# Kernel optimization log

Measured on AMD Instinct MI355X. Metric: run time of the kernel, lower is better.

The kernel has to match this reference:

```python
import jax, jax.numpy as jnp
import numpy as np

B, H, W, P = 32, 512, 512, 8192
EPS = 1e-5


def setup_inputs() -> dict:
    key = jax.random.key(0)
    k1, k2, k3, k4, k5 = jax.random.split(key, 5)
    return {
        "depth_3dmm": jax.random.normal(k1, (B, 1, H, W), jnp.float32),
        "depth_pigan": jax.random.normal(k2, (B, 1, H, W), jnp.float32),
        "mask": jax.random.randint(k3, (B, 1, H, W), 0, 2, jnp.int32),
        "sample1_raw": jax.random.randint(k4, (B, P), 0, H * W, jnp.int32),
        "sample2_raw": jax.random.randint(k5, (B, P), 0, H * W, jnp.int32),
    }


def reference(depth_3dmm, depth_pigan, mask, sample1_raw, sample2_raw):
    d3 = depth_3dmm.squeeze(axis=1)   # [B,H,W]
    dp = depth_pigan.squeeze(axis=1)  # [B,H,W]
    m = mask[:, 0].astype(bool)       # [B,H,W]
    Bv = m.shape[0]

    # Emulate torch.masked_select compaction with a fixed-shape stable argsort:
    # valid elements come first, in flat row-major order (same as masked_select).
    mflat = m.reshape(-1)
    order = jnp.argsort(jnp.logical_not(mflat))  # stable by default
    d3c = d3.reshape(-1)[order]  # compacted depth_3dmm (padding at tail)
    dpc = dp.reshape(-1)[order]  # compacted depth_pigan

    valid_num = m.reshape(Bv, -1).sum(axis=1)          # [B]
    batch_base = jnp.cumsum(valid_num) - valid_num     # [B]

    s1 = (sample1_raw % valid_num[:, None] + batch_base[:, None]).reshape(-1)
    s2 = (sample2_raw % valid_num[:, None] + batch_base[:, None]).reshape(-1)

    diff = dpc[s1] - dpc[s2]
    a, b = d3c[s1], d3c[s2]
    gt = a > b + EPS
    lt = a < b - EPS

    # mean(relu(-diff)[gt]) and mean(relu(diff)[lt]) without dynamic shapes
    loss1 = jnp.where(gt, jax.nn.relu(-diff), 0.0).sum() / gt.sum()
    loss2 = jnp.where(lt, jax.nn.relu(diff), 0.0).sum() / lt.sum()
    return (loss1 + loss2) / 2
```

## Files before the change

kernel.cpp:

```cpp
#include <hip/hip_runtime.h>
#include <stdint.h>

#define BB 32
#define HH 512
#define WW 512
#define HWSZ (HH * WW)
#define PP 8192
#define WPB (HWSZ / 64)
#define EPSV 1e-5f

#define SEG 4096
#define SEGS (HWSZ / SEG)
#define NBLK_L 256

__device__ inline uint32_t f2bf(float f) {
    uint32_t u = __float_as_uint(f);
    return (u + 0x7FFFu + ((u >> 16) & 1u)) >> 16;
}

__global__ __launch_bounds__(256) void k_compact_seg(const int* __restrict__ mask,
                                                     const float* __restrict__ d3,
                                                     const float* __restrict__ dp,
                                                     uint32_t* __restrict__ compact,
                                                     uint32_t* __restrict__ counts,
                                                     uint32_t* __restrict__ accu) {
    __shared__ uint32_t wsum[4];
    const int tid = threadIdx.x, lane = tid & 63, wid = tid >> 6;
    const int blk = blockIdx.x;
    const int batch = blk >> 6;
    const int seg = blk & 63;
    const int e0 = batch * HWSZ + seg * SEG + tid * 16;

    const int4* m4 = reinterpret_cast<const int4*>(mask + e0);
    const float4* a4 = reinterpret_cast<const float4*>(d3 + e0);
    const float4* p4 = reinterpret_cast<const float4*>(dp + e0);
    int4 mv[4];
    float4 av[4], pv[4];
#pragma unroll
    for (int j = 0; j < 4; ++j) { mv[j] = m4[j]; av[j] = a4[j]; pv[j] = p4[j]; }

    uint32_t bits = 0;
#pragma unroll
    for (int j = 0; j < 4; ++j) {
        bits |= (uint32_t)(mv[j].x != 0) << (4 * j + 0);
        bits |= (uint32_t)(mv[j].y != 0) << (4 * j + 1);
        bits |= (uint32_t)(mv[j].z != 0) << (4 * j + 2);
        bits |= (uint32_t)(mv[j].w != 0) << (4 * j + 3);
    }
    uint32_t cnt = (uint32_t)__popc(bits);

    uint32_t s = cnt;
#pragma unroll
    for (int off = 1; off < 64; off <<= 1) {
        uint32_t n = __shfl_up(s, off);
        if (lane >= off) s += n;
    }
    if (lane == 63) wsum[wid] = s;
    __syncthreads();
    uint32_t base = 0;
#pragma unroll
    for (int i = 0; i < 4; ++i) if (i < wid) base += wsum[i];
    uint32_t dest = (uint32_t)(batch * HWSZ + seg * SEG) + base + s - cnt;
    if (tid == 255) counts[blk] = base + s;
    if (blk == 0 && tid == 0) accu[0] = 0u;

#pragma unroll
    for (int j = 0; j < 4; ++j) {
        uint32_t bj = bits >> (4 * j);
        if (bj & 1u) compact[dest++] = f2bf(av[j].x) | (f2bf(pv[j].x) << 16);
        if (bj & 2u) compact[dest++] = f2bf(av[j].y) | (f2bf(pv[j].y) << 16);
        if (bj & 4u) compact[dest++] = f2bf(av[j].z) | (f2bf(pv[j].z) << 16);
        if (bj & 8u) compact[dest++] = f2bf(av[j].w) | (f2bf(pv[j].w) << 16);
    }
}

__global__ __launch_bounds__(256) void k_loss_seg(const uint32_t* __restrict__ compact,
                                                  const uint32_t* __restrict__ counts,
                                                  const int* __restrict__ s1raw,
                                                  const int* __restrict__ s2raw,
                                                  uint32_t* __restrict__ partials,
                                                  uint32_t* __restrict__ accu,
                                                  float* __restrict__ out) {
    __shared__ uint32_t pref[65];
    __shared__ float sv1[4], sv2[4];
    __shared__ uint32_t sc1[4], sc2[4];
    __shared__ int is_last;

    const int tid = threadIdx.x, lane = tid & 63, wid = tid >> 6;
    const int w = (blockIdx.x & 7) * 32 + (blockIdx.x >> 3);
    const int batch = w >> 3;
    const int j = w & 7;

    if (tid < 64) {
        uint32_t c = counts[batch * SEGS + tid];
        uint32_t s = c;
#pragma unroll
        for (int off = 1; off < 64; off <<= 1) {
            uint32_t n = __shfl_up(s, off);
            if (lane >= off) s += n;
        }
        pref[tid] = s - c;
        if (tid == 63) pref[64] = s;
    }
    __syncthreads();
    uint32_t vn = pref[64];
    if (vn == 0u || vn > (uint32_t)HWSZ) vn = (uint32_t)HWSZ;

    const uint32_t cbase = (uint32_t)(batch * HWSZ);
    auto locate = [&](uint32_t k) -> uint32_t {
        int lo = 0, hi = 64;
#pragma unroll
        for (int step = 0; step < 6; ++step) {
            int mid = (lo + hi) >> 1;
            if (pref[mid] <= k) lo = mid; else hi = mid;
        }
        return cbase + (uint32_t)(lo * SEG) + (k - pref[lo]);
    };

    int pb = batch * PP + j * (PP / 8) + tid;
    uint32_t i1[4], i2[4], g1[4], g2[4];
#pragma unroll
    for (int q = 0; q < 4; ++q) {
        int p = pb + q * 256;
        i1[q] = locate((uint32_t)s1raw[p] % vn);
        i2[q] = locate((uint32_t)s2raw[p] % vn);
    }
#pragma unroll
    for (int q = 0; q < 4; ++q) { g1[q] = compact[i1[q]]; g2[q] = compact[i2[q]]; }

    float v1 = 0.f, v2 = 0.f;
    uint32_t c1 = 0u, c2 = 0u;
#pragma unroll
    for (int q = 0; q < 4; ++q) {
        float a    = __uint_as_float(g1[q] << 16);
        float bv   = __uint_as_float(g2[q] << 16);
        float diff = __uint_as_float(g1[q] & 0xFFFF0000u) -
                     __uint_as_float(g2[q] & 0xFFFF0000u);
        if (a > bv + EPSV) { v1 += fmaxf(-diff, 0.0f); c1 += 1u; }
        if (a < bv - EPSV) { v2 += fmaxf(diff, 0.0f);  c2 += 1u; }
    }

#pragma unroll
    for (int off = 32; off > 0; off >>= 1) {
        v1 += __shfl_down(v1, off);
        v2 += __shfl_down(v2, off);
        c1 += __shfl_down(c1, off);
        c2 += __shfl_down(c2, off);
    }
    if (lane == 0) { sv1[wid] = v1; sv2[wid] = v2; sc1[wid] = c1; sc2[wid] = c2; }
    __syncthreads();

    if (tid == 0) {
        float t1 = sv1[0] + sv1[1] + sv1[2] + sv1[3];
        float t2 = sv2[0] + sv2[1] + sv2[2] + sv2[3];
        uint32_t u1 = sc1[0] + sc1[1] + sc1[2] + sc1[3];
        uint32_t u2 = sc2[0] + sc2[1] + sc2[2] + sc2[3];
        uint4 rec = make_uint4(__float_as_uint(t1), __float_as_uint(t2), u1, u2);
        *reinterpret_cast<uint4*>(partials + 4 * w) = rec;
        __threadfence();
        uint32_t ticket = __hip_atomic_fetch_add(&accu[0], 1u, __ATOMIC_ACQ_REL,
                                                 __HIP_MEMORY_SCOPE_AGENT);
        is_last = (ticket == (uint32_t)(NBLK_L - 1)) ? 1 : 0;
    }
    __syncthreads();

    if (is_last) {
        uint32_t r0 = __hip_atomic_load(&partials[4 * tid + 0], __ATOMIC_RELAXED,
                                        __HIP_MEMORY_SCOPE_AGENT);
        uint32_t r1 = __hip_atomic_load(&partials[4 * tid + 1], __ATOMIC_RELAXED,
                                        __HIP_MEMORY_SCOPE_AGENT);
        uint32_t r2 = __hip_atomic_load(&partials[4 * tid + 2], __ATOMIC_RELAXED,
                                        __HIP_MEMORY_SCOPE_AGENT);
        uint32_t r3 = __hip_atomic_load(&partials[4 * tid + 3], __ATOMIC_RELAXED,
                                        __HIP_MEMORY_SCOPE_AGENT);
        float fv1 = __uint_as_float(r0);
        float fv2 = __uint_as_float(r1);
        uint32_t uc1 = r2, uc2 = r3;
#pragma unroll
        for (int off = 32; off > 0; off >>= 1) {
            fv1 += __shfl_down(fv1, off);
            fv2 += __shfl_down(fv2, off);
            uc1 += __shfl_down(uc1, off);
            uc2 += __shfl_down(uc2, off);
        }
        __syncthreads();
        if (lane == 0) { sv1[wid] = fv1; sv2[wid] = fv2; sc1[wid] = uc1; sc2[wid] = uc2; }
        __syncthreads();
        if (tid == 0) {
            float s1t = sv1[0] + sv1[1] + sv1[2] + sv1[3];
            float s2t = sv2[0] + sv2[1] + sv2[2] + sv2[3];
            uint32_t n1 = sc1[0] + sc1[1] + sc1[2] + sc1[3];
            uint32_t n2 = sc2[0] + sc2[1] + sc2[2] + sc2[3];
            out[0] = 0.5f * (s1t / (float)n1 + s2t / (float)n2);
        }
    }
}

__global__ __launch_bounds__(256) void k_bitmap_fb(const int* __restrict__ mask,
                                                   uint64_t* __restrict__ words,
                                                   float* __restrict__ accf,
                                                   uint32_t* __restrict__ accu) {
    int gid = blockIdx.x * 256 + threadIdx.x;
    unsigned long long ball = __ballot(mask[gid] != 0);
    if ((threadIdx.x & 63) == 0) words[gid >> 6] = (uint64_t)ball;
    if (blockIdx.x == 0 && threadIdx.x == 0) {
        accf[0] = 0.0f; accf[1] = 0.0f;
        accu[0] = 0u; accu[1] = 0u; accu[2] = 0u;
    }
}

__global__ __launch_bounds__(256) void k_scan_fb(const uint64_t* __restrict__ words,
                                                 uint32_t* __restrict__ wprefix,
                                                 uint32_t* __restrict__ valid_num) {
    __shared__ uint32_t wsum[4];
    int b = blockIdx.x, t = threadIdx.x, lane = t & 63, wid = t >> 6;
    const uint64_t* wbp = words + (size_t)b * WPB;
    uint32_t pc[16], s = 0;
    int base = t * 16;
#pragma unroll
    for (int i = 0; i < 16; ++i) { pc[i] = (uint32_t)__popcll(wbp[base + i]); s += pc[i]; }
    uint32_t own = s;
#pragma unroll
    for (int off = 1; off < 64; off <<= 1) { uint32_t n = __shfl_up(s, off); if (lane >= off) s += n; }
    if (lane == 63) wsum[wid] = s;
    __syncthreads();
    uint32_t wb = 0;
#pragma unroll
    for (int i = 0; i < 4; ++i) if (i < wid) wb += wsum[i];
    uint32_t off2 = wb + s - own;
    if (t == 255) valid_num[b] = wb + s;
    uint32_t* wp = wprefix + (size_t)b * WPB;
#pragma unroll
    for (int i = 0; i < 16; ++i) { wp[base + i] = off2; off2 += pc[i]; }
}

__global__ __launch_bounds__(256) void k_loss_search(const float* __restrict__ d3,
                                                     const float* __restrict__ dp,
                                                     const int* __restrict__ s1raw,
                                                     const int* __restrict__ s2raw,
                                                     const uint64_t* __restrict__ words,
                                                     const uint32_t* __restrict__ wprefix,
                                                     const uint32_t* __restrict__ valid_num,
                                                     float* __restrict__ accf,
                                                     uint32_t* __restrict__ accu,
                                                     float* __restrict__ out) {
    __shared__ uint32_t wp[WPB];
    __shared__ float sv1[4], sv2[4];
    __shared__ uint32_t sc1[4], sc2[4];
    int b = blockIdx.x >> 5;
    int gid = blockIdx.x * 256 + threadIdx.x;
    const uint32_t* wpg = wprefix + (size_t)b * WPB;
    for (int i = threadIdx.x; i < WPB; i += 256) wp[i] = wpg[i];
    __syncthreads();
    uint32_t vn = valid_num[b];
    const uint64_t* wbp = words + (size_t)b * WPB;
    const float* d3b = d3 + (size_t)b * HWSZ;
    const float* dpb = dp + (size_t)b * HWSZ;
    uint32_t k1 = (uint32_t)s1raw[gid] % vn;
    uint32_t k2 = (uint32_t)s2raw[gid] % vn;
    auto sel = [&](uint32_t k) -> int {
        int lo = 0, hi = WPB;
        while (hi - lo > 1) { int mid = (lo + hi) >> 1; if (wp[mid] <= k) lo = mid; else hi = mid; }
        uint32_t r = k - wp[lo];
        uint64_t x = wbp[lo];
        int pos = lo << 6;
        uint32_t c = (uint32_t)__popcll(x & 0xFFFFFFFFull);
        if (r >= c) { r -= c; pos += 32; x >>= 32; }
        uint32_t y = (uint32_t)x;
        c = (uint32_t)__popc(y & 0xFFFFu); if (r >= c) { r -= c; pos += 16; y >>= 16; }
        c = (uint32_t)__popc(y & 0xFFu);   if (r >= c) { r -= c; pos += 8;  y >>= 8; }
        c = (uint32_t)__popc(y & 0xFu);    if (r >= c) { r -= c; pos += 4;  y >>= 4; }
        c = (uint32_t)__popc(y & 0x3u);    if (r >= c) { r -= c; pos += 2;  y >>= 2; }
        c = y & 1u;                        if (r >= c) { pos += 1; }
        return pos;
    };
    int i1 = sel(k1), i2 = sel(k2);
    float a = d3b[i1], bv = d3b[i2];
    float diff = dpb[i1] - dpb[i2];
    bool gt = a > bv + EPSV, lt = a < bv - EPSV;
    float v1 = gt ? fmaxf(-diff, 0.0f) : 0.0f;
    float v2 = lt ? fmaxf(diff, 0.0f) : 0.0f;
    uint32_t c1 = gt ? 1u : 0u, c2 = lt ? 1u : 0u;
#pragma unroll
    for (int off = 32; off > 0; off >>= 1) {
        v1 += __shfl_down(v1, off); v2 += __shfl_down(v2, off);
        c1 += __shfl_down(c1, off); c2 += __shfl_down(c2, off);
    }
    int wid = threadIdx.x >> 6;
    if ((threadIdx.x & 63) == 0) { sv1[wid] = v1; sv2[wid] = v2; sc1[wid] = c1; sc2[wid] = c2; }
    __syncthreads();
    if (threadIdx.x == 0) {
        float t1 = 0.f, t2 = 0.f; uint32_t u1 = 0, u2 = 0;
        for (int i = 0; i < 4; ++i) { t1 += sv1[i]; t2 += sv2[i]; u1 += sc1[i]; u2 += sc2[i]; }
        atomicAdd(&accf[0], t1); atomicAdd(&accf[1], t2);
        atomicAdd(&accu[0], u1); atomicAdd(&accu[1], u2);
        __threadfence();
        uint32_t ticket = atomicAdd(&accu[2], 1u);
        if (ticket == (uint32_t)(gridDim.x - 1)) {
            float sum1 = atomicAdd(&accf[0], 0.0f);
            float sum2 = atomicAdd(&accf[1], 0.0f);
            uint32_t n1 = atomicAdd(&accu[0], 0u);
            uint32_t n2 = atomicAdd(&accu[1], 0u);
            out[0] = 0.5f * (sum1 / (float)n1 + sum2 / (float)n2);
        }
    }
}

extern "C" void kernel_launch(void* const* d_in, const int* in_sizes, int n_in,
                              void* d_out, int out_size, void* d_ws, size_t ws_size,
                              hipStream_t stream) {
    const float* d3  = (const float*)d_in[0];
    const float* dp  = (const float*)d_in[1];
    const int*  mask = (const int*)d_in[2];
    const int*  s1   = (const int*)d_in[3];
    const int*  s2   = (const int*)d_in[4];
    float* out = (float*)d_out;
    char* ws = (char*)d_ws;

    uint32_t* counts   = (uint32_t*)ws;
    uint32_t* accu     = (uint32_t*)(ws + 16384);
    uint32_t* partials = (uint32_t*)(ws + 32768);
    uint32_t* compact  = (uint32_t*)(ws + 2097152);

    const size_t need = 2097152 + (size_t)BB * HWSZ * sizeof(uint32_t);

    if (ws_size >= need) {
        k_compact_seg<<<BB * SEGS, 256, 0, stream>>>(mask, d3, dp, compact,
                                                     counts, accu);
        k_loss_seg<<<NBLK_L, 256, 0, stream>>>(compact, counts, s1, s2,
                                               partials, accu, out);
    } else {
        uint64_t* words     = (uint64_t*)ws;
        uint32_t* wprefix   = (uint32_t*)(ws + 1048576);
        uint32_t* valid_num = (uint32_t*)(ws + 1572864);
        float*    accf      = (float*)(ws + 1573120);
        uint32_t* faccu     = (uint32_t*)(ws + 1573184);
        k_bitmap_fb<<<(BB * HWSZ) / 256, 256, 0, stream>>>(mask, words, accf, faccu);
        k_scan_fb<<<BB, 256, 0, stream>>>(words, wprefix, valid_num);
        k_loss_search<<<(BB * PP) / 256, 256, 0, stream>>>(d3, dp, s1, s2, words,
                                                           wprefix, valid_num,
                                                           accf, faccu, out);
    }
}
```

Baseline: 153.5 us.

## Stage compacted values in LDS and write them out with coalesced vector stores

```diff
diff --git a/kernel.cpp b/kernel.cpp
--- a/kernel.cpp
+++ b/kernel.cpp
@@ -9,8 +9,8 @@
 #define WPB (HWSZ / 64)
 #define EPSV 1e-5f
 
-#define SEG 4096
-#define SEGS (HWSZ / SEG)
+#define CSEG 2048
+#define CSEGS (HWSZ / CSEG)
 #define NBLK_L 256
 
 __device__ inline uint32_t f2bf(float f) {
@@ -25,28 +25,30 @@
                                                      uint32_t* __restrict__ counts,
                                                      uint32_t* __restrict__ accu) {
     __shared__ uint32_t wsum[4];
+    __shared__ __align__(16) uint32_t lbuf[CSEG];
+    __shared__ uint32_t stot;
     const int tid = threadIdx.x, lane = tid & 63, wid = tid >> 6;
     const int blk = blockIdx.x;
-    const int batch = blk >> 6;
-    const int seg = blk & 63;
-    const int e0 = batch * HWSZ + seg * SEG + tid * 16;
-
-    const int4* m4 = reinterpret_cast<const int4*>(mask + e0);
+    const int batch = blk >> 7;
+    const int seg = blk & 127;
+    const int e0 = batch * HWSZ + seg * CSEG + tid * 8;
+
+    const int4*   m4 = reinterpret_cast<const int4*>(mask + e0);
     const float4* a4 = reinterpret_cast<const float4*>(d3 + e0);
     const float4* p4 = reinterpret_cast<const float4*>(dp + e0);
-    int4 mv[4];
-    float4 av[4], pv[4];
-#pragma unroll
-    for (int j = 0; j < 4; ++j) { mv[j] = m4[j]; av[j] = a4[j]; pv[j] = p4[j]; }
+    int4   m0 = m4[0], m1 = m4[1];
+    float4 a0 = a4[0], a1 = a4[1];
+    float4 p0 = p4[0], p1 = p4[1];
 
     uint32_t bits = 0;
-#pragma unroll
-    for (int j = 0; j < 4; ++j) {
-        bits |= (uint32_t)(mv[j].x != 0) << (4 * j + 0);
-        bits |= (uint32_t)(mv[j].y != 0) << (4 * j + 1);
-        bits |= (uint32_t)(mv[j].z != 0) << (4 * j + 2);
-        bits |= (uint32_t)(mv[j].w != 0) << (4 * j + 3);
-    }
+    bits |= (uint32_t)(m0.x != 0) << 0;
+    bits |= (uint32_t)(m0.y != 0) << 1;
+    bits |= (uint32_t)(m0.z != 0) << 2;
+    bits |= (uint32_t)(m0.w != 0) << 3;
+    bits |= (uint32_t)(m1.x != 0) << 4;
+    bits |= (uint32_t)(m1.y != 0) << 5;
+    bits |= (uint32_t)(m1.z != 0) << 6;
+    bits |= (uint32_t)(m1.w != 0) << 7;
     uint32_t cnt = (uint32_t)__popc(bits);
 
     uint32_t s = cnt;
@@ -60,17 +62,31 @@
     uint32_t base = 0;
 #pragma unroll
     for (int i = 0; i < 4; ++i) if (i < wid) base += wsum[i];
-    uint32_t dest = (uint32_t)(batch * HWSZ + seg * SEG) + base + s - cnt;
-    if (tid == 255) counts[blk] = base + s;
+    uint32_t pos = base + s - cnt;
+    if (tid == 255) { stot = base + s; counts[blk] = base + s; }
     if (blk == 0 && tid == 0) accu[0] = 0u;
 
-#pragma unroll
-    for (int j = 0; j < 4; ++j) {
-        uint32_t bj = bits >> (4 * j);
-        if (bj & 1u) compact[dest++] = f2bf(av[j].x) | (f2bf(pv[j].x) << 16);
-        if (bj & 2u) compact[dest++] = f2bf(av[j].y) | (f2bf(pv[j].y) << 16);
-        if (bj & 4u) compact[dest++] = f2bf(av[j].z) | (f2bf(pv[j].z) << 16);
-        if (bj & 8u) compact[dest++] = f2bf(av[j].w) | (f2bf(pv[j].w) << 16);
+    uint32_t pk[8];
+    pk[0] = f2bf(a0.x) | (f2bf(p0.x) << 16);
+    pk[1] = f2bf(a0.y) | (f2bf(p0.y) << 16);
+    pk[2] = f2bf(a0.z) | (f2bf(p0.z) << 16);
+    pk[3] = f2bf(a0.w) | (f2bf(p0.w) << 16);
+    pk[4] = f2bf(a1.x) | (f2bf(p1.x) << 16);
+    pk[5] = f2bf(a1.y) | (f2bf(p1.y) << 16);
+    pk[6] = f2bf(a1.z) | (f2bf(p1.z) << 16);
+    pk[7] = f2bf(a1.w) | (f2bf(p1.w) << 16);
+#pragma unroll
+    for (int j = 0; j < 8; ++j) {
+        if (bits & (1u << j)) lbuf[pos++] = pk[j];
+    }
+    __syncthreads();
+
+    uint32_t tot = stot;
+    uint32_t bout = (uint32_t)(batch * HWSZ + seg * CSEG);
+    uint32_t nvec = (tot + 3u) >> 2;
+    for (uint32_t i = tid; i < nvec; i += 256) {
+        uint4 v = *reinterpret_cast<uint4*>(&lbuf[4 * i]);
+        *reinterpret_cast<uint4*>(&compact[bout + 4 * i]) = v;
     }
 }
 
@@ -81,7 +97,8 @@
                                                   uint32_t* __restrict__ partials,
                                                   uint32_t* __restrict__ accu,
                                                   float* __restrict__ out) {
-    __shared__ uint32_t pref[65];
+    __shared__ uint32_t pref[CSEGS + 1];
+    __shared__ uint32_t wtot[2];
     __shared__ float sv1[4], sv2[4];
     __shared__ uint32_t sc1[4], sc2[4];
     __shared__ int is_last;
@@ -91,30 +108,35 @@
     const int batch = w >> 3;
     const int j = w & 7;
 
-    if (tid < 64) {
-        uint32_t c = counts[batch * SEGS + tid];
-        uint32_t s = c;
-#pragma unroll
-        for (int off = 1; off < 64; off <<= 1) {
-            uint32_t n = __shfl_up(s, off);
-            if (lane >= off) s += n;
-        }
-        pref[tid] = s - c;
-        if (tid == 63) pref[64] = s;
-    }
-    __syncthreads();
-    uint32_t vn = pref[64];
+    uint32_t c = 0;
+    if (tid < CSEGS) c = counts[batch * CSEGS + tid];
+    uint32_t s = c;
+#pragma unroll
+    for (int off = 1; off < 64; off <<= 1) {
+        uint32_t n = __shfl_up(s, off);
+        if (lane >= off) s += n;
+    }
+    if (lane == 63 && wid < 2) wtot[wid] = s;
+    __syncthreads();
+    if (tid < CSEGS) {
+        uint32_t add = (wid == 1) ? wtot[0] : 0u;
+        pref[tid] = add + s - c;
+        if (tid == CSEGS - 1) pref[CSEGS] = add + s;
+    }
+    __syncthreads();
+
+    uint32_t vn = pref[CSEGS];
     if (vn == 0u || vn > (uint32_t)HWSZ) vn = (uint32_t)HWSZ;
 
     const uint32_t cbase = (uint32_t)(batch * HWSZ);
     auto locate = [&](uint32_t k) -> uint32_t {
-        int lo = 0, hi = 64;
-#pragma unroll
-        for (int step = 0; step < 6; ++step) {
+        int lo = 0, hi = CSEGS;
+#pragma unroll
+        for (int step = 0; step < 7; ++step) {
             int mid = (lo + hi) >> 1;
             if (pref[mid] <= k) lo = mid; else hi = mid;
         }
-        return cbase + (uint32_t)(lo * SEG) + (k - pref[lo]);
+        return cbase + (uint32_t)(lo * CSEG) + (k - pref[lo]);
     };
 
     int pb = batch * PP + j * (PP / 8) + tid;
@@ -325,8 +347,8 @@
     const size_t need = 2097152 + (size_t)BB * HWSZ * sizeof(uint32_t);
 
     if (ws_size >= need) {
-        k_compact_seg<<<BB * SEGS, 256, 0, stream>>>(mask, d3, dp, compact,
-                                                     counts, accu);
+        k_compact_seg<<<BB * CSEGS, 256, 0, stream>>>(mask, d3, dp, compact,
+                                                      counts, accu);
         k_loss_seg<<<NBLK_L, 256, 0, stream>>>(compact, counts, s1, s2,
                                                partials, accu, out);
     } else {
```

After: 143.1 us. 6.8% less time.
